# Kernel tuning notes

Hardware: AMD Instinct MI355X
Metric: run time of the kernel (lower is better)

Reference implementation:

```python
import jax, jax.numpy as jnp
import numpy as np
import math

H = 5120        # hidden_size
NH = 32         # num heads
HD = H // NH    # head_dim = 160
B = 1
S = 2048
TRAIN_SEQLEN = 8192
BASE = 10000.0


def _rotary_cos_sin(seq_len):
    # Eval-mode RotaryEmbedding: seq_len clamped to training_seqlen, NTK alpha + mscale (logN) scaling.
    eff = max(seq_len, TRAIN_SEQLEN)
    scale = eff / TRAIN_SEQLEN
    mscale = 1.0 if scale <= 1.0 else 0.1 * math.log(scale) + 1.0
    ntk_alpha = max(2 ** math.ceil(math.log(eff / 4096, 2) + 1) - 1, 1)
    base = BASE * ntk_alpha ** (HD / (HD - 2))
    inv_freq = 1.0 / base ** (np.arange(0, HD, 2, dtype=np.float64) / HD)
    t = np.arange(eff, dtype=np.float64)
    freqs = np.outer(t, inv_freq)              # [eff, HD/2]
    emb = np.concatenate([freqs, freqs], axis=-1)  # [eff, HD]
    cos = (mscale * np.cos(emb))[:seq_len].astype(np.float32)
    sin = (mscale * np.sin(emb))[:seq_len].astype(np.float32)
    return jnp.asarray(cos), jnp.asarray(sin)


def _rotate_half(x):
    x1, x2 = x[..., : HD // 2], x[..., HD // 2 :]
    return jnp.concatenate([-x2, x1], axis=-1)


def setup_inputs() -> dict:
    key = jax.random.key(0)
    ks = jax.random.split(key, 6)
    hidden_states = jax.random.normal(ks[0], (B, S, H), jnp.float32)
    residual = jax.random.normal(ks[1], (B, S, H), jnp.float32)
    # boolean causal mask, True = masked (matches masked_fill semantics)
    attention_mask = jnp.triu(jnp.ones((S, S), dtype=bool), k=1)[None, None]
    Wq = jax.random.normal(ks[2], (H, H), jnp.float32) * 0.02      # query: Linear(h, h, bias=False)
    Wkv = jax.random.normal(ks[3], (2 * H, H), jnp.float32) * 0.02  # key_value: Linear(h, 2h, bias=False)
    Wd = jax.random.normal(ks[4], (H, H), jnp.float32) * 0.02       # dense: Linear(h, h) with bias
    bd = jnp.zeros((H,), jnp.float32)
    return {
        "hidden_states": hidden_states,
        "residual": residual,
        "attention_mask": attention_mask,
        "Wq": Wq,
        "Wkv": Wkv,
        "Wd": Wd,
        "bd": bd,
    }


def reference(hidden_states, residual, attention_mask, Wq, Wkv, Wd, bd):
    b, s, h = hidden_states.shape
    # QKV projections (torch Linear: y = x @ W.T)
    q = jnp.einsum('bsh,oh->bso', hidden_states, Wq).reshape(b, s, NH, HD)
    kv = jnp.einsum('bsh,oh->bso', hidden_states, Wkv).reshape(b, s, NH, 2 * HD)
    k, v = kv[..., :HD], kv[..., HD:]
    # rotary embedding with logN mscale folded into cos/sin
    cos, sin = _rotary_cos_sin(s)               # [s, HD]
    cos = cos[None, :, None, :]
    sin = sin[None, :, None, :]
    q = q * cos + _rotate_half(q) * sin
    k = k * cos + _rotate_half(k) * sin
    inv_norm = 1.0 / math.sqrt(HD)
    scores = jnp.einsum('bqnd,bknd->bnqk', q, k) * inv_norm   # [b, nh, s, s]
    scores = jnp.where(attention_mask, jnp.finfo(scores.dtype).min, scores)
    probs = jax.nn.softmax(scores, axis=-1)
    # attention_dropout p=0.0 -> identity
    ctx = jnp.einsum('bnqk,bknd->bqnd', probs, v).reshape(b, s, h)
    out = ctx @ Wd.T + bd
    # dropout_add with hidden_dropout=0.0 (eval) -> residual + out
    return residual + out
```

## Files before the change

kernel.cpp:

```cpp
#include <hip/hip_runtime.h>
#include <cmath>

typedef unsigned short u16;
typedef unsigned int   u32;

using bf16x8 = __attribute__((ext_vector_type(8))) short;
using f32x4  = __attribute__((ext_vector_type(4))) float;

#define S_LEN 2048
#define NHEAD 32
#define HDIM  160
#define HID   5120
#define NQKV  15360

__device__ __forceinline__ f32x4 mfma16(bf16x8 a, bf16x8 b, f32x4 c) {
  return __builtin_amdgcn_mfma_f32_16x16x32_bf16(a, b, c, 0, 0, 0);
}

__device__ __forceinline__ u16 f2bf(float f) {
  u32 u = __builtin_bit_cast(u32, f);
  u += 0x7FFFu + ((u >> 16) & 1u);
  return (u16)(u >> 16);
}
__device__ __forceinline__ float bf2f(u16 h) {
  u32 u = ((u32)h) << 16;
  return __builtin_bit_cast(float, u);
}

__device__ __forceinline__ void gload16(const void* g, void* l) {
  __builtin_amdgcn_global_load_lds((const __attribute__((address_space(1))) void*)g,
                                   (__attribute__((address_space(3))) void*)l, 16, 0, 0);
}

__global__ void cvt_bf16_kernel(const float* __restrict__ in, u16* __restrict__ out, int n8) {
  int i = blockIdx.x * 256 + threadIdx.x;
  if (i >= n8) return;
  const float4* p = (const float4*)in + (size_t)i * 2;
  float4 a = p[0], b = p[1];
  uint4 o;
  o.x = (u32)f2bf(a.x) | ((u32)f2bf(a.y) << 16);
  o.y = (u32)f2bf(a.z) | ((u32)f2bf(a.w) << 16);
  o.z = (u32)f2bf(b.x) | ((u32)f2bf(b.y) << 16);
  o.w = (u32)f2bf(b.z) | ((u32)f2bf(b.w) << 16);
  ((uint4*)out)[i] = o;
}

__global__ void rope_table_kernel(float2* __restrict__ tab) {
  int i = blockIdx.x * 256 + threadIdx.x;
  if (i >= S_LEN * 80) return;
  int s = i / 80, j = i % 80;
  double base = 10000.0 * pow(3.0, 160.0 / 158.0);
  double invf = pow(base, -((double)(2 * j)) / 160.0);
  double ang  = fmod((double)s * invf, 6.283185307179586476925287);
  tab[i] = make_float2((float)cos(ang), (float)sin(ang));
}

__global__ void rope_apply_kernel(const u16* __restrict__ src, const float2* __restrict__ tab,
                                  u16* __restrict__ dst, int headStride, int rowStride) {
  int i = blockIdx.x * 256 + threadIdx.x;
  if (i >= S_LEN * NHEAD * 80) return;
  int dp = i % 80; int sh = i / 80; int h = sh % NHEAD; int s = sh / NHEAD;
  int d = 2 * dp;
  const u16* row = src + (size_t)s * rowStride + h * headStride;
  u32 q01 = *(const u32*)&row[d];
  u32 p01 = *(const u32*)&row[d < 80 ? d + 80 : d - 80];
  int j = (d < 80) ? d : d - 80;
  float2 cs0 = tab[s * 80 + j];
  float2 cs1 = tab[s * 80 + j + 1];
  float q0 = bf2f((u16)(q01 & 0xffff)), q1 = bf2f((u16)(q01 >> 16));
  float p0 = bf2f((u16)(p01 & 0xffff)), p1 = bf2f((u16)(p01 >> 16));
  float sgn = (d < 80) ? -1.f : 1.f;
  float o0 = q0 * cs0.x + sgn * p0 * cs0.y;
  float o1 = q1 * cs1.x + sgn * p1 * cs1.y;
  u32 o = (u32)f2bf(o0) | ((u32)f2bf(o1) << 16);
  *(u32*)&dst[((size_t)h * S_LEN + s) * HDIM + d] = o;
}

__global__ void vtrans_kernel(const u16* __restrict__ src, u16* __restrict__ Vt, int rowStride) {
  __shared__ u16 T[HDIM][72];
  int h = blockIdx.y; int s0 = blockIdx.x * 64; int tid = threadIdx.x;
  for (int i = tid; i < 64 * 80; i += 256) {
    int s = i / 80, dp = i % 80;
    u32 v = *(const u32*)&src[(size_t)(s0 + s) * rowStride + h * 320 + 2 * dp];
    T[2 * dp][s]     = (u16)(v & 0xffff);
    T[2 * dp + 1][s] = (u16)(v >> 16);
  }
  __syncthreads();
  for (int i = tid; i < HDIM * 32; i += 256) {
    int d = i / 32, sp = i % 32;
    u32 v = (u32)T[d][2 * sp] | ((u32)T[d][2 * sp + 1] << 16);
    *(u32*)&Vt[((size_t)h * HDIM + d) * S_LEN + s0 + 2 * sp] = v;
  }
}

template<int EPI>
__global__ __launch_bounds__(512, 2) void gemm256(
    const u16* __restrict__ A, const u16* __restrict__ Bm, void* __restrict__ Cout,
    int M, int N, int K, const float* __restrict__ bias, const float* __restrict__ resid)
{
  __shared__ u16 As[2][2][8192];
  __shared__ u16 Bs[2][2][8192];
  int tid = threadIdx.x;
  int w = tid >> 6, l = tid & 63, l15 = l & 15, l4 = l >> 4;
  int wr = w >> 2, wc = w & 3;

  int nbx = gridDim.x;
  int nwg = nbx * gridDim.y;
  int lin = blockIdx.y * nbx + blockIdx.x;
  int cpx = nwg >> 3;
  int swz = (lin & 7) * cpx + (lin >> 3);
  int bm = (swz / nbx) * 256, bn = (swz % nbx) * 256;

  int srow = tid >> 2;
  int scol = ((tid & 3) * 8) ^ ((srow & 8) ? 16 : 0);
  const u16* gA0 = A  + (size_t)(bm +       srow) * K + scol;
  const u16* gA1 = A  + (size_t)(bm + 128 + srow) * K + scol;
  const u16* gB0 = Bm + (size_t)(bn +       srow) * K + scol;
  const u16* gB1 = Bm + (size_t)(bn + 128 + srow) * K + scol;
  int dstoff = w * 512;

  f32x4 acc[8][4];
#pragma unroll
  for (int i = 0; i < 8; i++)
#pragma unroll
    for (int j = 0; j < 4; j++) acc[i][j] = f32x4{0.f, 0.f, 0.f, 0.f};

  int cA = (l4 * 8) ^ ((l15 & 8) ? 16 : 0);
  const int NT = K >> 6;

  auto STAGE = [&](int kt, int p) {
    int k0 = kt << 6;
    gload16(gA0 + k0,      &As[p][0][dstoff]);
    gload16(gA0 + k0 + 32, &As[p][0][4096 + dstoff]);
    gload16(gA1 + k0,      &As[p][1][dstoff]);
    gload16(gA1 + k0 + 32, &As[p][1][4096 + dstoff]);
    gload16(gB0 + k0,      &Bs[p][0][dstoff]);
    gload16(gB0 + k0 + 32, &Bs[p][0][4096 + dstoff]);
    gload16(gB1 + k0,      &Bs[p][1][dstoff]);
    gload16(gB1 + k0 + 32, &Bs[p][1][4096 + dstoff]);
  };

  STAGE(0, 0);
  for (int kt = 0; kt < NT; ++kt) {
    int p = kt & 1;
    if (kt + 1 < NT) {
      STAGE(kt + 1, p ^ 1);
      asm volatile("s_waitcnt vmcnt(8)" ::: "memory");
    } else {
      asm volatile("s_waitcnt vmcnt(0)" ::: "memory");
    }
    __builtin_amdgcn_s_barrier();

    const u16* Ah = &As[p][wr][0];
    const u16* Bh = &Bs[p][wc >> 1][0];
    int bcol = (wc & 1) * 64;
#pragma unroll
    for (int kk = 0; kk < 2; ++kk) {
      bf16x8 aF[8], bF[4];
#pragma unroll
      for (int mi = 0; mi < 8; ++mi)
        aF[mi] = *(const bf16x8*)&Ah[kk * 4096 + (mi * 16 + l15) * 32 + cA];
#pragma unroll
      for (int ni = 0; ni < 4; ++ni)
        bF[ni] = *(const bf16x8*)&Bh[kk * 4096 + (bcol + ni * 16 + l15) * 32 + cA];
      __builtin_amdgcn_s_setprio(1);
#pragma unroll
      for (int mi = 0; mi < 8; ++mi)
#pragma unroll
        for (int ni = 0; ni < 4; ++ni)
          acc[mi][ni] = mfma16(aF[mi], bF[ni], acc[mi][ni]);
      __builtin_amdgcn_s_setprio(0);
    }
    __builtin_amdgcn_s_barrier();
  }

#pragma unroll
  for (int mi = 0; mi < 8; ++mi)
#pragma unroll
    for (int ni = 0; ni < 4; ++ni) {
      int row0 = bm + wr * 128 + mi * 16 + l4 * 4;
      int col  = bn + wc * 64 + ni * 16 + l15;
      if (EPI == 0) {
        u16* C = (u16*)Cout;
#pragma unroll
        for (int r = 0; r < 4; r++) C[(size_t)(row0 + r) * N + col] = f2bf(acc[mi][ni][r]);
      } else {
        float* C = (float*)Cout;
        float b = bias[col];
#pragma unroll
        for (int r = 0; r < 4; r++) {
          size_t idx = (size_t)(row0 + r) * N + col;
          C[idx] = acc[mi][ni][r] + b + resid[idx];
        }
      }
    }
}

__global__ __launch_bounds__(512, 4) void attn_kernel(
    const u16* __restrict__ Qr, const u16* __restrict__ Kr,
    const u16* __restrict__ Vt, u16* __restrict__ ctx)
{
  int lin = blockIdx.x;
  int qx = 15 - (lin >> 5);
  int h  = lin & 31;
  int q0 = qx * 128;
  int tid = threadIdx.x;
  int w = tid >> 6, l = tid & 63, l15 = l & 15, l4 = l >> 4;
  int qb = q0 + w * 16;

  __shared__ u16 Ks[64][164];
  __shared__ u16 Vs[160][68];
  __shared__ u16 Plds[8][16][68];

  const u16* Qh = Qr + (size_t)h * S_LEN * HDIM;
  const u16* Kh = Kr + (size_t)h * S_LEN * HDIM;
  const u16* Vh = Vt + (size_t)h * HDIM * S_LEN;

  bf16x8 aQ[5];
#pragma unroll
  for (int kc = 0; kc < 5; kc++)
    aQ[kc] = *(const bf16x8*)&Qh[(size_t)(qb + l15) * HDIM + kc * 32 + l4 * 8];

  f32x4 accO[10];
#pragma unroll
  for (int dt = 0; dt < 10; dt++) accO[dt] = f32x4{0.f, 0.f, 0.f, 0.f};
  float mrun[4], lrun[4];
#pragma unroll
  for (int r = 0; r < 4; r++) { mrun[r] = -1e30f; lrun[r] = 0.f; }

  const float c2 = 0.07905694150420949f * 1.44269504088896f;
  int Tend = 2 * qx + 2;

  {
    uint4 rg[5];
#pragma unroll
    for (int i = 0; i < 5; i++) {
      int u = tid + 512 * i;
      if (u < 1280) { int row = u / 20, c = u % 20;
        rg[i] = *(const uint4*)&Kh[(size_t)row * HDIM + c * 8]; }
      else { int v = u - 1280; int row = v >> 3, c = v & 7;
        rg[i] = *(const uint4*)&Vh[(size_t)row * S_LEN + c * 8]; }
    }
#pragma unroll
    for (int i = 0; i < 5; i++) {
      int u = tid + 512 * i;
      if (u < 1280) { int row = u / 20, c = u % 20; *(uint4*)&Ks[row][c * 8] = rg[i]; }
      else { int v = u - 1280; int row = v >> 3, c = v & 7; *(uint4*)&Vs[row][c * 8] = rg[i]; }
    }
  }
  __syncthreads();

  for (int t = 0; t < Tend; ++t) {
    int k0 = t * 64;
    bool more = (t + 1 < Tend);
    uint4 rg[5];
    if (more) {
      int k1 = k0 + 64;
#pragma unroll
      for (int i = 0; i < 5; i++) {
        int u = tid + 512 * i;
        if (u < 1280) { int row = u / 20, c = u % 20;
          rg[i] = *(const uint4*)&Kh[(size_t)(k1 + row) * HDIM + c * 8]; }
        else { int v = u - 1280; int row = v >> 3, c = v & 7;
          rg[i] = *(const uint4*)&Vh[(size_t)row * S_LEN + k1 + c * 8]; }
      }
    }

    if (k0 <= qb + 15) {
      f32x4 s_[4];
#pragma unroll
      for (int nt = 0; nt < 4; nt++) s_[nt] = f32x4{0.f, 0.f, 0.f, 0.f};

#pragma unroll
      for (int kc = 0; kc < 5; kc++) {
        bf16x8 bK[4];
#pragma unroll
        for (int nt = 0; nt < 4; nt++)
          bK[nt] = *(const bf16x8*)&Ks[nt * 16 + l15][kc * 32 + l4 * 8];
#pragma unroll
        for (int nt = 0; nt < 4; nt++) s_[nt] = mfma16(aQ[kc], bK[nt], s_[nt]);
      }

      if (k0 + 63 > qb) {
#pragma unroll
        for (int nt = 0; nt < 4; nt++)
#pragma unroll
          for (int r = 0; r < 4; r++) {
            int kk = k0 + nt * 16 + l15;
            int qq = qb + l4 * 4 + r;
            if (kk > qq) s_[nt][r] = -1e30f;
          }
      }

      float sf[4];
#pragma unroll
      for (int r = 0; r < 4; r++) {
        float v = fmaxf(fmaxf(s_[0][r], s_[1][r]), fmaxf(s_[2][r], s_[3][r]));
#pragma unroll
        for (int m = 1; m <= 8; m <<= 1) v = fmaxf(v, __shfl_xor(v, m));
        float mnew = fmaxf(mrun[r], v);
        sf[r] = exp2f((mrun[r] - mnew) * c2);
        mrun[r] = mnew;
      }
      float rsum[4] = {0.f, 0.f, 0.f, 0.f};
#pragma unroll
      for (int nt = 0; nt < 4; nt++)
#pragma unroll
        for (int r = 0; r < 4; r++) {
          float p = exp2f((s_[nt][r] - mrun[r]) * c2);
          s_[nt][r] = p;
          rsum[r] += p;
        }
#pragma unroll
      for (int r = 0; r < 4; r++) {
        float v = rsum[r];
#pragma unroll
        for (int m = 1; m <= 8; m <<= 1) v += __shfl_xor(v, m);
        lrun[r] = lrun[r] * sf[r] + v;
      }
#pragma unroll
      for (int dt = 0; dt < 10; dt++)
#pragma unroll
        for (int r = 0; r < 4; r++) accO[dt][r] *= sf[r];
#pragma unroll
      for (int nt = 0; nt < 4; nt++)
#pragma unroll
        for (int r = 0; r < 4; r++)
          Plds[w][l4 * 4 + r][nt * 16 + l15] = f2bf(s_[nt][r]);

#pragma unroll
      for (int kc = 0; kc < 2; kc++) {
        bf16x8 aP = *(const bf16x8*)&Plds[w][l15][kc * 32 + l4 * 8];
        bf16x8 bV[10];
#pragma unroll
        for (int dt = 0; dt < 10; dt++)
          bV[dt] = *(const bf16x8*)&Vs[dt * 16 + l15][kc * 32 + l4 * 8];
#pragma unroll
        for (int dt = 0; dt < 10; dt++)
          accO[dt] = mfma16(aP, bV[dt], accO[dt]);
      }
    }

    __syncthreads();
    if (more) {
#pragma unroll
      for (int i = 0; i < 5; i++) {
        int u = tid + 512 * i;
        if (u < 1280) { int row = u / 20, c = u % 20; *(uint4*)&Ks[row][c * 8] = rg[i]; }
        else { int v = u - 1280; int row = v >> 3, c = v & 7; *(uint4*)&Vs[row][c * 8] = rg[i]; }
      }
    }
    __syncthreads();
  }

  float inv[4];
#pragma unroll
  for (int r = 0; r < 4; r++) inv[r] = 1.0f / lrun[r];
#pragma unroll
  for (int dt = 0; dt < 10; dt++)
#pragma unroll
    for (int r = 0; r < 4; r++) {
      int q = qb + l4 * 4 + r;
      ctx[(size_t)q * HID + h * HDIM + dt * 16 + l15] = f2bf(accO[dt][r] * inv[r]);
    }
}

extern "C" void kernel_launch(void* const* d_in, const int* in_sizes, int n_in,
                              void* d_out, int out_size, void* d_ws, size_t ws_size,
                              hipStream_t stream) {
  const float* hs    = (const float*)d_in[0];
  const float* resid = (const float*)d_in[1];
  const float* Wq  = (const float*)d_in[3];
  const float* Wkv = (const float*)d_in[4];
  const float* Wd  = (const float*)d_in[5];
  const float* bd  = (const float*)d_in[6];
  float* out = (float*)d_out;

  char* ws = (char*)d_ws;
  const size_t SH = (size_t)S_LEN * HID;
  u16* Xb     = (u16*)(ws);                        size_t off = SH * 2;
  u16* Wqkvb  = (u16*)(ws + off);                  off += (size_t)3 * HID * HID * 2;
  u16* Wdb    = (u16*)(ws + off);                  off += (size_t)HID * HID * 2;
  u16* QKVraw = (u16*)(ws + off);                  off += (size_t)S_LEN * NQKV * 2;
  u16* Qr     = (u16*)(ws + off);                  off += SH * 2;
  u16* Kr     = (u16*)(ws + off);                  off += SH * 2;
  u16* Vt     = (u16*)(ws + off);                  off += SH * 2;
  u16* ctx    = (u16*)(ws + off);                  off += SH * 2;
  float2* tab = (float2*)(ws + off);               off += (size_t)S_LEN * 80 * 8;

  cvt_bf16_kernel<<<(int)(SH / 8 / 256), 256, 0, stream>>>(hs, Xb, (int)(SH / 8));
  cvt_bf16_kernel<<<HID * HID / 8 / 256, 256, 0, stream>>>(Wq, Wqkvb, HID * HID / 8);
  cvt_bf16_kernel<<<2 * HID * HID / 8 / 256, 256, 0, stream>>>(Wkv, Wqkvb + (size_t)HID * HID, 2 * HID * HID / 8);
  cvt_bf16_kernel<<<HID * HID / 8 / 256, 256, 0, stream>>>(Wd, Wdb, HID * HID / 8);

  rope_table_kernel<<<(S_LEN * 80 + 255) / 256, 256, 0, stream>>>(tab);

  gemm256<0><<<dim3(NQKV / 256, S_LEN / 256), 512, 0, stream>>>(
      Xb, Wqkvb, QKVraw, S_LEN, NQKV, HID, nullptr, nullptr);

  rope_apply_kernel<<<S_LEN * NHEAD * 80 / 256, 256, 0, stream>>>(QKVraw, tab, Qr, HDIM, NQKV);
  rope_apply_kernel<<<S_LEN * NHEAD * 80 / 256, 256, 0, stream>>>(QKVraw + HID, tab, Kr, 2 * HDIM, NQKV);
  vtrans_kernel<<<dim3(S_LEN / 64, NHEAD), 256, 0, stream>>>(QKVraw + HID + HDIM, Vt, NQKV);

  attn_kernel<<<512, 512, 0, stream>>>(Qr, Kr, Vt, ctx);

  gemm256<1><<<dim3(HID / 256, S_LEN / 256), 512, 0, stream>>>(
      ctx, Wdb, out, S_LEN, HID, HID, bd, resid);
}
```

Before: 1.016 ms.

## Retile output GEMM, rebalance attention blocks, add MFMA priority and lighter barriers

The output projection moves from the 256x256 GEMM to a new 128x128-tile GEMM with an XCD-aware swizzle, giving 640 workgroups instead of 160 so more CUs stay busy. The attention grid mapping now runs the heavy causal blocks first for half the grid and the light blocks first for the other half, which changes load balance. MFMA sections are wrapped in s_setprio, and __syncthreads is replaced by s_barrier plus an explicit LDS waitcnt. The rope table now computes inverse frequencies once per block in shared memory and uses float cosf/sinf, which may slightly change precision. The new GEMM loads with a single LDS buffer and no double buffering, so global-load latency may be exposed.

```diff
diff --git a/kernel.cpp b/kernel.cpp
--- a/kernel.cpp
+++ b/kernel.cpp
@@ -46,13 +46,19 @@
 }
 
 __global__ void rope_table_kernel(float2* __restrict__ tab) {
-  int i = blockIdx.x * 256 + threadIdx.x;
-  if (i >= S_LEN * 80) return;
-  int s = i / 80, j = i % 80;
-  double base = 10000.0 * pow(3.0, 160.0 / 158.0);
-  double invf = pow(base, -((double)(2 * j)) / 160.0);
-  double ang  = fmod((double)s * invf, 6.283185307179586476925287);
-  tab[i] = make_float2((float)cos(ang), (float)sin(ang));
+  __shared__ double invf_s[80];
+  int tid = threadIdx.x;
+  if (tid < 80) {
+    double base = 10000.0 * pow(3.0, 160.0 / 158.0);
+    invf_s[tid] = pow(base, -((double)(2 * tid)) / 160.0);
+  }
+  __syncthreads();
+  for (int i = blockIdx.x * 256 + tid; i < S_LEN * 80; i += gridDim.x * 256) {
+    int s = i / 80, j = i % 80;
+    double ang = fmod((double)s * invf_s[j], 6.283185307179586476925287);
+    float a = (float)ang;
+    tab[i] = make_float2(cosf(a), sinf(a));
+  }
 }
 
 __global__ void rope_apply_kernel(const u16* __restrict__ src, const float2* __restrict__ tab,
@@ -196,13 +202,80 @@
     }
 }
 
+template<int EPI>
+__global__ __launch_bounds__(256, 2) void gemm_bt(
+    const u16* __restrict__ A, const u16* __restrict__ Bm, void* __restrict__ Cout,
+    int M, int N, int K, const float* __restrict__ bias, const float* __restrict__ resid)
+{
+  int tid = threadIdx.x;
+  int wv = tid >> 6, l = tid & 63, l15 = l & 15, l4 = l >> 4;
+  int nbx = gridDim.x;
+  int nwg = nbx * gridDim.y;
+  int lin = blockIdx.y * nbx + blockIdx.x;
+  int cpx = nwg >> 3;
+  int swz = (lin & 7) * cpx + (lin >> 3);
+  int bm = (swz / nbx) * 128, bn = (swz % nbx) * 128;
+
+  __shared__ u16 As[128 * 32], Bs[128 * 32];
+  f32x4 acc[4][4];
+#pragma unroll
+  for (int i = 0; i < 4; i++)
+#pragma unroll
+    for (int j = 0; j < 4; j++) acc[i][j] = f32x4{0.f, 0.f, 0.f, 0.f};
+
+  int wm = (wv >> 1) * 64, wn = (wv & 1) * 64;
+  const u16* gA = A + (size_t)(bm + (tid >> 2)) * K + (tid & 3) * 8;
+  const u16* gB = Bm + (size_t)(bn + (tid >> 2)) * K + (tid & 3) * 8;
+  u16* ldsA = As + wv * 16 * 32;
+  u16* ldsB = Bs + wv * 16 * 32;
+
+  for (int k0 = 0; k0 < K; k0 += 32) {
+    __syncthreads();
+    gload16(gA + k0, ldsA);
+    gload16(gA + (size_t)64 * K + k0, ldsA + 64 * 32);
+    gload16(gB + k0, ldsB);
+    gload16(gB + (size_t)64 * K + k0, ldsB + 64 * 32);
+    __syncthreads();
+    bf16x8 af[4], bfr[4];
+#pragma unroll
+    for (int i = 0; i < 4; i++) af[i] = *(const bf16x8*)&As[(wm + i * 16 + l15) * 32 + l4 * 8];
+#pragma unroll
+    for (int i = 0; i < 4; i++) bfr[i] = *(const bf16x8*)&Bs[(wn + i * 16 + l15) * 32 + l4 * 8];
+#pragma unroll
+    for (int mi = 0; mi < 4; mi++)
+#pragma unroll
+      for (int ni = 0; ni < 4; ni++) acc[mi][ni] = mfma16(af[mi], bfr[ni], acc[mi][ni]);
+  }
+
+#pragma unroll
+  for (int mi = 0; mi < 4; mi++)
+#pragma unroll
+    for (int ni = 0; ni < 4; ni++) {
+      int row0 = bm + wm + mi * 16 + l4 * 4;
+      int col  = bn + wn + ni * 16 + l15;
+      if (EPI == 0) {
+        u16* C = (u16*)Cout;
+#pragma unroll
+        for (int r = 0; r < 4; r++) C[(size_t)(row0 + r) * N + col] = f2bf(acc[mi][ni][r]);
+      } else {
+        float* C = (float*)Cout;
+        float b = bias[col];
+#pragma unroll
+        for (int r = 0; r < 4; r++) {
+          size_t idx = (size_t)(row0 + r) * N + col;
+          C[idx] = acc[mi][ni][r] + b + resid[idx];
+        }
+      }
+    }
+}
+
 __global__ __launch_bounds__(512, 4) void attn_kernel(
     const u16* __restrict__ Qr, const u16* __restrict__ Kr,
     const u16* __restrict__ Vt, u16* __restrict__ ctx)
 {
   int lin = blockIdx.x;
-  int qx = 15 - (lin >> 5);
   int h  = lin & 31;
+  int qx = (lin < 256) ? (15 - (lin >> 5)) : ((lin - 256) >> 5);
   int q0 = qx * 128;
   int tid = threadIdx.x;
   int w = tid >> 6, l = tid & 63, l15 = l & 15, l4 = l >> 4;
@@ -277,8 +350,10 @@
 #pragma unroll
         for (int nt = 0; nt < 4; nt++)
           bK[nt] = *(const bf16x8*)&Ks[nt * 16 + l15][kc * 32 + l4 * 8];
+        __builtin_amdgcn_s_setprio(1);
 #pragma unroll
         for (int nt = 0; nt < 4; nt++) s_[nt] = mfma16(aQ[kc], bK[nt], s_[nt]);
+        __builtin_amdgcn_s_setprio(0);
       }
 
       if (k0 + 63 > qb) {
@@ -335,13 +410,15 @@
 #pragma unroll
         for (int dt = 0; dt < 10; dt++)
           bV[dt] = *(const bf16x8*)&Vs[dt * 16 + l15][kc * 32 + l4 * 8];
+        __builtin_amdgcn_s_setprio(1);
 #pragma unroll
         for (int dt = 0; dt < 10; dt++)
           accO[dt] = mfma16(aP, bV[dt], accO[dt]);
-      }
-    }
-
-    __syncthreads();
+        __builtin_amdgcn_s_setprio(0);
+      }
+    }
+
+    __builtin_amdgcn_s_barrier();
     if (more) {
 #pragma unroll
       for (int i = 0; i < 5; i++) {
@@ -349,8 +426,9 @@
         if (u < 1280) { int row = u / 20, c = u % 20; *(uint4*)&Ks[row][c * 8] = rg[i]; }
         else { int v = u - 1280; int row = v >> 3, c = v & 7; *(uint4*)&Vs[row][c * 8] = rg[i]; }
       }
-    }
-    __syncthreads();
+      asm volatile("s_waitcnt lgkmcnt(0)" ::: "memory");
+    }
+    __builtin_amdgcn_s_barrier();
   }
 
   float inv[4];
@@ -393,7 +471,7 @@
   cvt_bf16_kernel<<<2 * HID * HID / 8 / 256, 256, 0, stream>>>(Wkv, Wqkvb + (size_t)HID * HID, 2 * HID * HID / 8);
   cvt_bf16_kernel<<<HID * HID / 8 / 256, 256, 0, stream>>>(Wd, Wdb, HID * HID / 8);
 
-  rope_table_kernel<<<(S_LEN * 80 + 255) / 256, 256, 0, stream>>>(tab);
+  rope_table_kernel<<<64, 256, 0, stream>>>(tab);
 
   gemm256<0><<<dim3(NQKV / 256, S_LEN / 256), 512, 0, stream>>>(
       Xb, Wqkvb, QKVraw, S_LEN, NQKV, HID, nullptr, nullptr);
@@ -404,6 +482,6 @@
 
   attn_kernel<<<512, 512, 0, stream>>>(Qr, Kr, Vt, ctx);
 
-  gemm256<1><<<dim3(HID / 256, S_LEN / 256), 512, 0, stream>>>(
+  gemm_bt<1><<<dim3(HID / 128, S_LEN / 128), 256, 0, stream>>>(
       ctx, Wdb, out, S_LEN, HID, HID, bd, resid);
 }
```

Result: no change. 1.008 ms (-0.8%).
